# Kernel optimization log

Measured on AMD Instinct MI355X. Metric: run time of the kernel, lower is better.

The kernel has to match this reference:

```python
import jax, jax.numpy as jnp
import numpy as np
import math


def _rel_pos_tables(W):
    # continuous relative coords table: [(2W-1), (2W-1), 2]
    c = np.arange(-(W - 1), W, dtype=np.float32)
    table = np.stack(np.meshgrid(c, c, indexing='ij'), axis=-1)  # [2W-1,2W-1,2]
    table = table / (W - 1)
    table = table * 8.0
    table = np.sign(table) * np.log2(np.abs(table) + 1.0) / math.log2(8.0)
    # relative position index: [W*W, W*W]
    coords = np.stack(np.meshgrid(np.arange(W), np.arange(W), indexing='ij'))  # [2,W,W]
    flat = coords.reshape(2, -1)  # [2, W*W]
    rel = flat[:, :, None] - flat[:, None, :]  # [2, N, N]
    rel = rel.transpose(1, 2, 0).copy()
    rel[:, :, 0] += W - 1
    rel[:, :, 1] += W - 1
    rel[:, :, 0] *= 2 * W - 1
    idx = rel.sum(-1)  # [N, N]
    return jnp.asarray(table), jnp.asarray(idx, dtype=jnp.int32)


def setup_inputs() -> dict:
    key = jax.random.key(0)
    ks = jax.random.split(key, 10)
    dim, W, H = 512, 8, 16
    N = W * W
    B_, nW = 2048, 256
    s = 0.02
    inp = {
        'x': jax.random.normal(ks[0], (B_, N, dim), jnp.float32),
        'mask': jax.random.normal(ks[1], (nW, N, N), jnp.float32),
        'qkv_w': jax.random.normal(ks[2], (dim, 3 * dim), jnp.float32) * s,
        'qkv_b': jnp.zeros((3 * dim,), jnp.float32),
        'logit_scale': jnp.full((H, 1, 1), math.log(10.0), jnp.float32),
        'cpb_w1': jax.random.normal(ks[3], (2, 512), jnp.float32) * s,
        'cpb_b1': jnp.zeros((512,), jnp.float32),
        'cpb_w2': jax.random.normal(ks[4], (512, H), jnp.float32) * s,
        'proj_w': jax.random.normal(ks[5], (dim, dim), jnp.float32) * s,
        'proj_b': jnp.zeros((dim,), jnp.float32),
        'window_size': W,
        'num_heads': H,
    }
    return inp


def reference(x, mask, qkv_w, qkv_b, logit_scale, cpb_w1, cpb_b1, cpb_w2,
              proj_w, proj_b, window_size, num_heads):
    B_, N, C = x.shape
    H = num_heads
    hd = C // H

    qkv = (x @ qkv_w + qkv_b).reshape(B_, N, 3, H, hd)
    qkv = jnp.transpose(qkv, (2, 0, 3, 1, 4))  # [3, B_, H, N, hd]
    q, k, v = qkv[0], qkv[1], qkv[2]

    # cosine attention: L2-normalize q, k (eps matches F.normalize)
    q = q / jnp.clip(jnp.linalg.norm(q, axis=-1, keepdims=True), 1e-12)
    k = k / jnp.clip(jnp.linalg.norm(k, axis=-1, keepdims=True), 1e-12)

    attn = jnp.einsum('bhnd,bhmd->bhnm', q, k)
    scale = jnp.exp(jnp.minimum(logit_scale, math.log(1.0 / 0.01)))  # [H,1,1]
    attn = attn * scale[None]

    # continuous relative position bias
    table, idx = _rel_pos_tables(window_size)
    t = jax.nn.relu(table @ cpb_w1 + cpb_b1) @ cpb_w2  # [2W-1, 2W-1, H]
    t = t.reshape(-1, H)
    bias = t[idx.reshape(-1)].reshape(N, N, H)
    bias = 16.0 * jax.nn.sigmoid(jnp.transpose(bias, (2, 0, 1)))  # [H, N, N]
    attn = attn + bias[None]

    # mask add: [nW, N, N]
    nW = mask.shape[0]
    attn = attn.reshape(B_ // nW, nW, H, N, N) + mask[None, :, None]
    attn = attn.reshape(B_, H, N, N)

    attn = jax.nn.softmax(attn, axis=-1)
    out = jnp.einsum('bhnm,bhmd->bhnd', attn, v)
    out = jnp.transpose(out, (0, 2, 1, 3)).reshape(B_, N, C)
    out = out @ proj_w + proj_b
    return out
```

## Files before the change

kernel.cpp:

```cpp
#include <hip/hip_runtime.h>
#include <hip/hip_bf16.h>
#include <stdint.h>

typedef __attribute__((ext_vector_type(8))) short short8;
typedef __attribute__((ext_vector_type(8))) _Float16 half8;
typedef __attribute__((ext_vector_type(4))) float f32x4;

__device__ __forceinline__ unsigned short f2h(float f) {
  union { _Float16 h; unsigned short u; } c;
  c.h = (_Float16)f;
  return c.u;
}
__device__ __forceinline__ float h2f(unsigned short u) {
  union { _Float16 h; unsigned short u; } c;
  c.u = u;
  return (float)c.h;
}
__device__ __forceinline__ void gload_lds16(const void* g, void* l) {
  __builtin_amdgcn_global_load_lds(
      (const __attribute__((address_space(1))) unsigned int*)g,
      (__attribute__((address_space(3))) unsigned int*)l, 16, 0, 0);
}


__global__ __launch_bounds__(256) void cast_f16(const float* __restrict__ in,
                                                unsigned short* __restrict__ out) {
  const size_t total = (size_t)131072 * 512 / 8;
  size_t stride = (size_t)gridDim.x * 256;
  for (size_t i = blockIdx.x * 256 + threadIdx.x; i < total; i += stride) {
    f32x4 f0 = *(const f32x4*)(in + i * 8);
    f32x4 f1 = *(const f32x4*)(in + i * 8 + 4);
    short8 o;
#pragma unroll
    for (int e = 0; e < 4; e++) {
      o[e] = (short)f2h(f0[e]);
      o[4 + e] = (short)f2h(f1[e]);
    }
    *(short8*)(out + i * 8) = o;
  }
}

__global__ __launch_bounds__(256) void transpose_cast(const float* __restrict__ in,
                                                      unsigned short* __restrict__ out,
                                                      int K, int N) {
  __shared__ float tile[32][33];
  int nb = N / 32;
  int bx = blockIdx.x % nb, by = blockIdx.x / nb;
  int tx = threadIdx.x & 31, ty = threadIdx.x >> 5;
#pragma unroll
  for (int r = 0; r < 32; r += 8)
    tile[ty + r][tx] = in[(size_t)(by * 32 + ty + r) * N + bx * 32 + tx];
  __syncthreads();
#pragma unroll
  for (int r = 0; r < 32; r += 8)
    out[(size_t)(bx * 32 + ty + r) * K + by * 32 + tx] = f2h(tile[tx][ty + r]);
}

__device__ __forceinline__ float cpb_coord(int a) {
  float v = (float)(a - 7) * (8.0f / 7.0f);
  float s = (v > 0.f) ? 1.f : ((v < 0.f) ? -1.f : 0.f);
  return s * log2f(fabsf(v) + 1.f) * (1.f / 3.f);
}

__global__ __launch_bounds__(64) void cpb_mlp(const float* __restrict__ w1,
                                              const float* __restrict__ b1,
                                              const float* __restrict__ w2,
                                              float* __restrict__ t_out) {
  int e = blockIdx.x;
  int dy = e / 15, dx = e % 15;
  float in0 = cpb_coord(dy), in1 = cpb_coord(dx);
  float acc[16];
#pragma unroll
  for (int o = 0; o < 16; ++o) acc[o] = 0.f;
  for (int u = threadIdx.x; u < 512; u += 64) {
    float hsum = fmaxf(in0 * w1[u] + in1 * w1[512 + u] + b1[u], 0.f);
#pragma unroll
    for (int o = 0; o < 16; ++o) acc[o] += hsum * w2[u * 16 + o];
  }
#pragma unroll
  for (int o = 0; o < 16; ++o) {
    float v = acc[o];
    v += __shfl_xor(v, 1);  v += __shfl_xor(v, 2);  v += __shfl_xor(v, 4);
    v += __shfl_xor(v, 8);  v += __shfl_xor(v, 16); v += __shfl_xor(v, 32);
    acc[o] = v;
  }
  if (threadIdx.x == 0)
#pragma unroll
    for (int o = 0; o < 16; ++o) t_out[e * 16 + o] = acc[o];
}

__global__ __launch_bounds__(256) void bias_kernel(const float* __restrict__ t,
                                                   float* __restrict__ bias) {
  int idx = blockIdx.x * 256 + threadIdx.x;
  int j = idx & 63, i = (idx >> 6) & 63, h = idx >> 12;
  int dy = (i >> 3) - (j >> 3) + 7;
  int dx = (i & 7) - (j & 7) + 7;
  float v = t[(dy * 15 + dx) * 16 + h];
  bias[idx] = 16.f / (1.f + expf(-v));
}

__global__ __launch_bounds__(256) void qkv_gemm(const unsigned short* __restrict__ xh,
                                               const unsigned short* __restrict__ Wt,
                                               const float* __restrict__ bvec,
                                               unsigned short* __restrict__ qout,
                                               unsigned short* __restrict__ kout,
                                               unsigned short* __restrict__ vout) {
  __shared__ __align__(16) short smem[16384];
  const int bid = (blockIdx.x & 7) * 1536 + (blockIdx.x >> 3);
  const int nt = bid % 12;
  const int mt = bid / 12;
  const int m0 = mt * 128, n0 = nt * 128;
  const int t = threadIdx.x;
  const int l = t & 63, w = t >> 6;
  const int wm = w >> 1, wn = w & 1;
  const int fr = l & 15, fg = l >> 4;
  const int sch = t & 3;

  f32x4 acc[4][4];
#pragma unroll
  for (int i = 0; i < 4; i++)
#pragma unroll
    for (int j = 0; j < 4; j++) acc[i][j] = f32x4{0.f, 0.f, 0.f, 0.f};

  auto STAGE = [&](int bsel, int k0) {
#pragma unroll
    for (int it = 0; it < 2; ++it) {
      int flat = it * 256 + t;
      int row = flat >> 2;
      gload_lds16(xh + (size_t)(m0 + row) * 512 + k0 + sch * 8,
                  &smem[bsel * 4096 + flat * 8]);
      gload_lds16(Wt + (size_t)(n0 + row) * 512 + k0 + sch * 8,
                  &smem[8192 + bsel * 4096 + flat * 8]);
    }
  };

  STAGE(0, 0);
  __syncthreads();
  int cur = 0;
  for (int k0 = 0; k0 < 512; k0 += 32) {
    if (k0 + 32 < 512) STAGE(cur ^ 1, k0 + 32);
    half8 af[4], bfr[4];
#pragma unroll
    for (int i = 0; i < 4; i++)
      af[i] = *(half8*)&smem[cur * 4096 + (wm * 64 + i * 16 + fr) * 32 + fg * 8];
#pragma unroll
    for (int j = 0; j < 4; j++)
      bfr[j] = *(half8*)&smem[8192 + cur * 4096 + (wn * 64 + j * 16 + fr) * 32 + fg * 8];
#pragma unroll
    for (int i = 0; i < 4; i++)
#pragma unroll
      for (int j = 0; j < 4; j++)
        acc[i][j] = __builtin_amdgcn_mfma_f32_16x16x32_f16(af[i], bfr[j], acc[i][j], 0, 0, 0);
    __syncthreads();
    cur ^= 1;
  }

#pragma unroll
  for (int j = 0; j < 4; j++) {
    int col = wn * 64 + j * 16 + fr;
    float bb = bvec[n0 + col];
#pragma unroll
    for (int i = 0; i < 4; i++) {
      int row0 = wm * 64 + i * 16 + fg * 4;
#pragma unroll
      for (int r = 0; r < 4; r++)
        smem[(row0 + r) * 128 + col] = (short)f2h(acc[i][j][r] + bb);
    }
  }
  __syncthreads();
  unsigned short* dst;
  int coloff;
  if (nt < 4)      { dst = qout; coloff = n0; }
  else if (nt < 8) { dst = kout; coloff = n0 - 512; }
  else             { dst = vout; coloff = n0 - 1024; }
#pragma unroll
  for (int it = 0; it < 8; ++it) {
    int flat = it * 256 + t;
    int row = flat >> 4, c16 = flat & 15;
    *(short8*)(dst + (size_t)(m0 + row) * 512 + coloff + c16 * 8) =
        *(short8*)&smem[row * 128 + c16 * 8];
  }
}

__global__ __launch_bounds__(256) void attn_kernel(const unsigned short* __restrict__ qws,
                                                   const unsigned short* __restrict__ kws,
                                                   const unsigned short* __restrict__ vws,
                                                   const float* __restrict__ bias,
                                                   const float* __restrict__ mask,
                                                   const float* __restrict__ logit_scale,
                                                   unsigned short* __restrict__ aout) {
  const int blk = (blockIdx.x & 7) * 4096 + (blockIdx.x >> 3);
  const int h = blk & 15;
  const int b = blk >> 4;
  const int wmi = b & 255;
  const int t = threadIdx.x, l = t & 63, w = t >> 6;

  __shared__ __align__(16) short qs[64 * 32], ks[64 * 32];
  __shared__ __align__(16) short vt[32 * 72];
  __shared__ __align__(16) short plds[4 * 16 * 72];
  __shared__ float invs[64];

  const float scale = __expf(fminf(logit_scale[h], 4.6051702f));

  {
    const int r = t >> 2, c4 = t & 3;
    {
      uint4 raw = *(const uint4*)(qws + (size_t)(b * 64 + r) * 512 + h * 32 + c4 * 8);
      unsigned int rr[4] = {raw.x, raw.y, raw.z, raw.w};
      float f[8];
#pragma unroll
      for (int e = 0; e < 4; e++) {
        f[2 * e]     = h2f((unsigned short)(rr[e] & 0xffff));
        f[2 * e + 1] = h2f((unsigned short)(rr[e] >> 16));
      }
      float ss = 0.f;
#pragma unroll
      for (int e = 0; e < 8; e++) ss += f[e] * f[e];
      ss += __shfl_xor(ss, 1);
      ss += __shfl_xor(ss, 2);
      float inv = 1.f / fmaxf(sqrtf(ss), 1e-12f);
      short8 o;
#pragma unroll
      for (int e = 0; e < 8; e++) o[e] = (short)f2h(f[e] * inv);
      *(short8*)&qs[r * 32 + c4 * 8] = o;
    }
    {
      uint4 raw = *(const uint4*)(kws + (size_t)(b * 64 + r) * 512 + h * 32 + c4 * 8);
      unsigned int rr[4] = {raw.x, raw.y, raw.z, raw.w};
      float f[8];
#pragma unroll
      for (int e = 0; e < 4; e++) {
        f[2 * e]     = h2f((unsigned short)(rr[e] & 0xffff));
        f[2 * e + 1] = h2f((unsigned short)(rr[e] >> 16));
      }
      float ss = 0.f;
#pragma unroll
      for (int e = 0; e < 8; e++) ss += f[e] * f[e];
      ss += __shfl_xor(ss, 1);
      ss += __shfl_xor(ss, 2);
      float inv = 1.f / fmaxf(sqrtf(ss), 1e-12f);
      short8 o;
#pragma unroll
      for (int e = 0; e < 8; e++) o[e] = (short)f2h(f[e] * inv);
      *(short8*)&ks[r * 32 + c4 * 8] = o;
    }
    {
      uint4 raw = *(const uint4*)(vws + (size_t)(b * 64 + r) * 512 + h * 32 + c4 * 8);
      unsigned int rr[4] = {raw.x, raw.y, raw.z, raw.w};
#pragma unroll
      for (int e2 = 0; e2 < 4; e2++) {
        vt[(c4 * 8 + 2 * e2 + 0) * 72 + r] = (short)(rr[e2] & 0xffff);
        vt[(c4 * 8 + 2 * e2 + 1) * 72 + r] = (short)(rr[e2] >> 16);
      }
    }
  }
  __syncthreads();

  const int fr = l & 15, fg = l >> 4;
  half8 bq = *(half8*)&qs[(w * 16 + fr) * 32 + fg * 8];

  f32x4 st[4];
#pragma unroll
  for (int kt = 0; kt < 4; kt++) {
    half8 ak = *(half8*)&ks[(kt * 16 + fr) * 32 + fg * 8];
    st[kt] = __builtin_amdgcn_mfma_f32_16x16x32_f16(ak, bq, f32x4{0.f, 0.f, 0.f, 0.f}, 0, 0, 0);
  }
  const int q = w * 16 + fr;
  const int kbase = fg * 4;
  float sv[16];
  float mx = -1e30f;
#pragma unroll
  for (int kt = 0; kt < 4; kt++) {
    f32x4 b4 = *(const f32x4*)&bias[(size_t)(h * 64 + q) * 64 + kt * 16 + kbase];
    f32x4 m4 = *(const f32x4*)&mask[(size_t)(wmi * 64 + q) * 64 + kt * 16 + kbase];
#pragma unroll
    for (int j = 0; j < 4; j++) {
      float xv = st[kt][j] * scale + b4[j] + m4[j];
      sv[kt * 4 + j] = xv;
      mx = fmaxf(mx, xv);
    }
  }
  mx = fmaxf(mx, __shfl_xor(mx, 16));
  mx = fmaxf(mx, __shfl_xor(mx, 32));
  float sum = 0.f;
#pragma unroll
  for (int i2 = 0; i2 < 16; i2++) {
    float p = __expf(sv[i2] - mx);
    sv[i2] = p;
    sum += p;
  }
  sum += __shfl_xor(sum, 16);
  sum += __shfl_xor(sum, 32);

  short* pl = &plds[w * 16 * 72];
#pragma unroll
  for (int kt = 0; kt < 4; kt++)
#pragma unroll
    for (int j = 0; j < 4; j += 2) {
      unsigned int pack = (unsigned int)f2h(sv[kt * 4 + j]) |
                          ((unsigned int)f2h(sv[kt * 4 + j + 1]) << 16);
      *(unsigned int*)&pl[fr * 72 + kt * 16 + kbase + j] = pack;
    }
  if (fg == 0) invs[q] = 1.f / sum;
  __syncthreads();

  half8 pa0 = *(half8*)&pl[fr * 72 + fg * 8];
  half8 pa1 = *(half8*)&pl[fr * 72 + 32 + fg * 8];
#pragma unroll
  for (int nt2 = 0; nt2 < 2; nt2++) {
    half8 bv0 = *(half8*)&vt[(nt2 * 16 + fr) * 72 + fg * 8];
    half8 bv1 = *(half8*)&vt[(nt2 * 16 + fr) * 72 + 32 + fg * 8];
    f32x4 o = f32x4{0.f, 0.f, 0.f, 0.f};
    o = __builtin_amdgcn_mfma_f32_16x16x32_f16(pa0, bv0, o, 0, 0, 0);
    o = __builtin_amdgcn_mfma_f32_16x16x32_f16(pa1, bv1, o, 0, 0, 0);
    const int qo = w * 16 + fg * 4;
    const int hd = nt2 * 16 + fr;
#pragma unroll
    for (int r2 = 0; r2 < 4; r2++) {
      float vv = o[r2] * invs[qo + r2];
      qs[(qo + r2) * 32 + hd] = (short)f2h(vv);
    }
  }
  __syncthreads();
  {
    const int row = t >> 2, c = t & 3;
    *(short8*)(aout + (size_t)(b * 64 + row) * 512 + h * 32 + c * 8) =
        *(short8*)&qs[row * 32 + c * 8];
  }
}

__global__ __launch_bounds__(256) void proj_gemm(const unsigned short* __restrict__ A,
                                                 const unsigned short* __restrict__ Wt,
                                                 const float* __restrict__ bvec,
                                                 float* __restrict__ out) {
  __shared__ __align__(16) short smem[16384];
  const int bid = (blockIdx.x & 7) * 512 + (blockIdx.x >> 3);
  const int nt = bid & 3;
  const int mt = bid >> 2;
  const int m0 = mt * 128, n0 = nt * 128;
  const int t = threadIdx.x;
  const int l = t & 63, w = t >> 6;
  const int wm = w >> 1, wn = w & 1;
  const int fr = l & 15, fg = l >> 4;
  const int sch = t & 3;

  f32x4 acc[4][4];
#pragma unroll
  for (int i = 0; i < 4; i++)
#pragma unroll
    for (int j = 0; j < 4; j++) acc[i][j] = f32x4{0.f, 0.f, 0.f, 0.f};

  auto STAGE = [&](int bsel, int k0) {
#pragma unroll
    for (int it = 0; it < 2; ++it) {
      int flat = it * 256 + t;
      int row = flat >> 2;
      gload_lds16(A + (size_t)(m0 + row) * 512 + k0 + sch * 8,
                  &smem[bsel * 4096 + flat * 8]);
      gload_lds16(Wt + (size_t)(n0 + row) * 512 + k0 + sch * 8,
                  &smem[8192 + bsel * 4096 + flat * 8]);
    }
  };

  STAGE(0, 0);
  __syncthreads();
  int cur = 0;
  for (int k0 = 0; k0 < 512; k0 += 32) {
    if (k0 + 32 < 512) STAGE(cur ^ 1, k0 + 32);
    half8 af[4], bfr[4];
#pragma unroll
    for (int i = 0; i < 4; i++)
      af[i] = *(half8*)&smem[cur * 4096 + (wm * 64 + i * 16 + fr) * 32 + fg * 8];
#pragma unroll
    for (int j = 0; j < 4; j++)
      bfr[j] = *(half8*)&smem[8192 + cur * 4096 + (wn * 64 + j * 16 + fr) * 32 + fg * 8];
#pragma unroll
    for (int i = 0; i < 4; i++)
#pragma unroll
      for (int j = 0; j < 4; j++)
        acc[i][j] = __builtin_amdgcn_mfma_f32_16x16x32_f16(af[i], bfr[j], acc[i][j], 0, 0, 0);
    __syncthreads();
    cur ^= 1;
  }

  float* bounce = (float*)smem;
#pragma unroll
  for (int half = 0; half < 2; ++half) {
    if (wm == half) {
#pragma unroll
      for (int j = 0; j < 4; j++) {
        int col = wn * 64 + j * 16 + fr;
        float bb = bvec[n0 + col];
#pragma unroll
        for (int i = 0; i < 4; i++) {
          int row0 = i * 16 + fg * 4;
#pragma unroll
          for (int r = 0; r < 4; r++)
            bounce[(row0 + r) * 128 + col] = acc[i][j][r] + bb;
        }
      }
    }
    __syncthreads();
#pragma unroll
    for (int it = 0; it < 8; ++it) {
      int flat = it * 256 + t;
      int row = flat >> 5, c4 = flat & 31;
      *(f32x4*)(out + (size_t)(m0 + half * 64 + row) * 512 + n0 + c4 * 4) =
          *(f32x4*)&bounce[row * 128 + c4 * 4];
    }
    __syncthreads();
  }
}

extern "C" void kernel_launch(void* const* d_in, const int* in_sizes, int n_in,
                              void* d_out, int out_size, void* d_ws, size_t ws_size,
                              hipStream_t stream) {
  const float* x           = (const float*)d_in[0];
  const float* mask        = (const float*)d_in[1];
  const float* qkv_w       = (const float*)d_in[2];
  const float* qkv_b       = (const float*)d_in[3];
  const float* logit_scale = (const float*)d_in[4];
  const float* cpb_w1      = (const float*)d_in[5];
  const float* cpb_b1      = (const float*)d_in[6];
  const float* cpb_w2      = (const float*)d_in[7];
  const float* proj_w      = (const float*)d_in[8];
  const float* proj_b      = (const float*)d_in[9];
  (void)in_sizes; (void)n_in; (void)out_size; (void)ws_size;

  char* p = (char*)d_ws;
  unsigned short* Wqkv_t  = (unsigned short*)p; p += (size_t)1536 * 512 * 2;
  unsigned short* Wproj_t = (unsigned short*)p; p += (size_t)512 * 512 * 2;
  float* t_cpb            = (float*)p;          p += (size_t)225 * 16 * 4;
  float* biasb            = (float*)p;          p += (size_t)16 * 64 * 64 * 4;
  unsigned short* xh      = (unsigned short*)p; p += (size_t)131072 * 512 * 2;
  unsigned short* qbuf    = (unsigned short*)p; p += (size_t)131072 * 512 * 2;
  unsigned short* kbuf    = (unsigned short*)p; p += (size_t)131072 * 512 * 2;
  unsigned short* vbuf    = (unsigned short*)p; p += (size_t)131072 * 512 * 2;
  unsigned short* abuf    = (unsigned short*)p; p += (size_t)131072 * 512 * 2;

  cast_f16<<<2048, 256, 0, stream>>>(x, xh);
  transpose_cast<<<768, 256, 0, stream>>>(qkv_w, Wqkv_t, 512, 1536);
  transpose_cast<<<256, 256, 0, stream>>>(proj_w, Wproj_t, 512, 512);
  cpb_mlp<<<225, 64, 0, stream>>>(cpb_w1, cpb_b1, cpb_w2, t_cpb);
  bias_kernel<<<256, 256, 0, stream>>>(t_cpb, biasb);
  qkv_gemm<<<12288, 256, 0, stream>>>(xh, Wqkv_t, qkv_b, qbuf, kbuf, vbuf);
  attn_kernel<<<32768, 256, 0, stream>>>(qbuf, kbuf, vbuf, biasb, mask, logit_scale, abuf);
  proj_gemm<<<4096, 256, 0, stream>>>(abuf, Wproj_t, proj_b, (float*)d_out);
}
```

Before: 747.0 us.

## Enlarge QKV GEMM tiles to 256x256 with 512 threads and K=64 stages

```diff
diff --git a/kernel.cpp b/kernel.cpp
--- a/kernel.cpp
+++ b/kernel.cpp
@@ -99,86 +99,107 @@
   bias[idx] = 16.f / (1.f + expf(-v));
 }
 
-__global__ __launch_bounds__(256) void qkv_gemm(const unsigned short* __restrict__ xh,
-                                               const unsigned short* __restrict__ Wt,
-                                               const float* __restrict__ bvec,
-                                               unsigned short* __restrict__ qout,
-                                               unsigned short* __restrict__ kout,
-                                               unsigned short* __restrict__ vout) {
-  __shared__ __align__(16) short smem[16384];
-  const int bid = (blockIdx.x & 7) * 1536 + (blockIdx.x >> 3);
-  const int nt = bid % 12;
-  const int mt = bid / 12;
-  const int m0 = mt * 128, n0 = nt * 128;
+__global__ __launch_bounds__(512, 2) void qkv_gemm(const unsigned short* __restrict__ xh,
+                                                   const unsigned short* __restrict__ Wt,
+                                                   const float* __restrict__ bvec,
+                                                   unsigned short* __restrict__ qout,
+                                                   unsigned short* __restrict__ kout,
+                                                   unsigned short* __restrict__ vout) {
+  __shared__ __align__(16) short smem[65536];
+  const int bid = (blockIdx.x & 7) * 384 + (blockIdx.x >> 3);
+  const int nt = bid % 6;
+  const int mt = bid / 6;
+  const int m0 = mt * 256, n0 = nt * 256;
   const int t = threadIdx.x;
-  const int l = t & 63, w = t >> 6;
-  const int wm = w >> 1, wn = w & 1;
+  const int l = t & 63, wid = t >> 6;
+  const int wm = wid >> 2, wn = wid & 3;
   const int fr = l & 15, fg = l >> 4;
-  const int sch = t & 3;
-
-  f32x4 acc[4][4];
-#pragma unroll
-  for (int i = 0; i < 4; i++)
+
+  f32x4 acc[8][4];
+#pragma unroll
+  for (int i = 0; i < 8; i++)
 #pragma unroll
     for (int j = 0; j < 4; j++) acc[i][j] = f32x4{0.f, 0.f, 0.f, 0.f};
 
-  auto STAGE = [&](int bsel, int k0) {
-#pragma unroll
-    for (int it = 0; it < 2; ++it) {
-      int flat = it * 256 + t;
-      int row = flat >> 2;
-      gload_lds16(xh + (size_t)(m0 + row) * 512 + k0 + sch * 8,
-                  &smem[bsel * 4096 + flat * 8]);
-      gload_lds16(Wt + (size_t)(n0 + row) * 512 + k0 + sch * 8,
-                  &smem[8192 + bsel * 4096 + flat * 8]);
+  auto STAGE = [&](int bsel, int kt) {
+#pragma unroll
+    for (int it = 0; it < 4; ++it) {
+      int flat = it * 512 + t;
+      int row = flat >> 3, c = flat & 7;
+      gload_lds16(xh + (size_t)(m0 + row) * 512 + kt * 64 + c * 8,
+                  &smem[bsel * 16384 + row * 64 + c * 8]);
+      gload_lds16(Wt + (size_t)(n0 + row) * 512 + kt * 64 + c * 8,
+                  &smem[32768 + bsel * 16384 + row * 64 + c * 8]);
     }
   };
 
   STAGE(0, 0);
-  __syncthreads();
+  __builtin_amdgcn_sched_barrier(0);
+  asm volatile("s_waitcnt vmcnt(0)" ::: "memory");
+  __builtin_amdgcn_sched_barrier(0);
+  __builtin_amdgcn_s_barrier();
+  __builtin_amdgcn_sched_barrier(0);
+
   int cur = 0;
-  for (int k0 = 0; k0 < 512; k0 += 32) {
-    if (k0 + 32 < 512) STAGE(cur ^ 1, k0 + 32);
-    half8 af[4], bfr[4];
-#pragma unroll
-    for (int i = 0; i < 4; i++)
-      af[i] = *(half8*)&smem[cur * 4096 + (wm * 64 + i * 16 + fr) * 32 + fg * 8];
-#pragma unroll
-    for (int j = 0; j < 4; j++)
-      bfr[j] = *(half8*)&smem[8192 + cur * 4096 + (wn * 64 + j * 16 + fr) * 32 + fg * 8];
-#pragma unroll
-    for (int i = 0; i < 4; i++)
-#pragma unroll
-      for (int j = 0; j < 4; j++)
-        acc[i][j] = __builtin_amdgcn_mfma_f32_16x16x32_f16(af[i], bfr[j], acc[i][j], 0, 0, 0);
-    __syncthreads();
+  for (int kt = 0; kt < 8; ++kt) {
+    if (kt < 7) STAGE(cur ^ 1, kt + 1);
+    __builtin_amdgcn_sched_barrier(0);
+    {
+      const short* Ab = &smem[cur * 16384];
+      const short* Bb = &smem[32768 + cur * 16384];
+      half8 bfr[4][2];
+#pragma unroll
+      for (int j = 0; j < 4; ++j)
+#pragma unroll
+        for (int kk = 0; kk < 2; ++kk)
+          bfr[j][kk] = *(const half8*)&Bb[(wn * 64 + j * 16 + fr) * 64 + kk * 32 + fg * 8];
+#pragma unroll
+      for (int i = 0; i < 8; ++i) {
+        half8 a0 = *(const half8*)&Ab[(wm * 128 + i * 16 + fr) * 64 + fg * 8];
+        half8 a1 = *(const half8*)&Ab[(wm * 128 + i * 16 + fr) * 64 + 32 + fg * 8];
+#pragma unroll
+        for (int j = 0; j < 4; ++j) {
+          acc[i][j] = __builtin_amdgcn_mfma_f32_16x16x32_f16(a0, bfr[j][0], acc[i][j], 0, 0, 0);
+          acc[i][j] = __builtin_amdgcn_mfma_f32_16x16x32_f16(a1, bfr[j][1], acc[i][j], 0, 0, 0);
+        }
+      }
+    }
+    __builtin_amdgcn_sched_barrier(0);
+    asm volatile("s_waitcnt vmcnt(0)" ::: "memory");
+    __builtin_amdgcn_sched_barrier(0);
+    __builtin_amdgcn_s_barrier();
+    __builtin_amdgcn_sched_barrier(0);
     cur ^= 1;
   }
 
-#pragma unroll
-  for (int j = 0; j < 4; j++) {
-    int col = wn * 64 + j * 16 + fr;
-    float bb = bvec[n0 + col];
-#pragma unroll
-    for (int i = 0; i < 4; i++) {
-      int row0 = wm * 64 + i * 16 + fg * 4;
-#pragma unroll
-      for (int r = 0; r < 4; r++)
-        smem[(row0 + r) * 128 + col] = (short)f2h(acc[i][j][r] + bb);
-    }
-  }
-  __syncthreads();
   unsigned short* dst;
   int coloff;
-  if (nt < 4)      { dst = qout; coloff = n0; }
-  else if (nt < 8) { dst = kout; coloff = n0 - 512; }
-  else             { dst = vout; coloff = n0 - 1024; }
-#pragma unroll
-  for (int it = 0; it < 8; ++it) {
-    int flat = it * 256 + t;
-    int row = flat >> 4, c16 = flat & 15;
-    *(short8*)(dst + (size_t)(m0 + row) * 512 + coloff + c16 * 8) =
-        *(short8*)&smem[row * 128 + c16 * 8];
+  if (nt < 2)      { dst = qout; coloff = nt * 256; }
+  else if (nt < 4) { dst = kout; coloff = (nt - 2) * 256; }
+  else             { dst = vout; coloff = (nt - 4) * 256; }
+#pragma unroll
+  for (int hh = 0; hh < 2; ++hh) {
+    if (hh) __syncthreads();
+    if (wm == hh) {
+#pragma unroll
+      for (int i = 0; i < 8; ++i)
+#pragma unroll
+        for (int j = 0; j < 4; ++j) {
+          int col = wn * 64 + j * 16 + fr;
+          float bb = bvec[n0 + col];
+#pragma unroll
+          for (int r = 0; r < 4; ++r)
+            smem[(i * 16 + fg * 4 + r) * 256 + col] = (short)f2h(acc[i][j][r] + bb);
+        }
+    }
+    __syncthreads();
+#pragma unroll
+    for (int it = 0; it < 8; ++it) {
+      int flat = it * 512 + t;
+      int row = flat >> 5, c32 = flat & 31;
+      *(short8*)(dst + (size_t)(m0 + hh * 128 + row) * 512 + coloff + c32 * 8) =
+          *(short8*)&smem[row * 256 + c32 * 8];
+    }
   }
 }
 
@@ -443,7 +464,7 @@
   transpose_cast<<<256, 256, 0, stream>>>(proj_w, Wproj_t, 512, 512);
   cpb_mlp<<<225, 64, 0, stream>>>(cpb_w1, cpb_b1, cpb_w2, t_cpb);
   bias_kernel<<<256, 256, 0, stream>>>(t_cpb, biasb);
-  qkv_gemm<<<12288, 256, 0, stream>>>(xh, Wqkv_t, qkv_b, qbuf, kbuf, vbuf);
+  qkv_gemm<<<3072, 512, 0, stream>>>(xh, Wqkv_t, qkv_b, qbuf, kbuf, vbuf);
   attn_kernel<<<32768, 256, 0, stream>>>(qbuf, kbuf, vbuf, biasb, mask, logit_scale, abuf);
   proj_gemm<<<4096, 256, 0, stream>>>(abuf, Wproj_t, proj_b, (float*)d_out);
 }
```

After: 737.2 us. Within noise of the previous version (-1.3%).
